# Performance work log

Measured on AMD Instinct MI355X. Metric: run time of the kernel, lower is better.

The kernel has to match this reference:

```python
import jax, jax.numpy as jnp
import numpy as np

NUM_HEADS = 16
EPS = 1e-6
CHUNK = 128  # chunk length for exact chunked-recurrent causal linear attention


def setup_inputs() -> dict:
    key = jax.random.key(0)
    ks = jax.random.split(key, 6)
    B, T, E = 4, 2048, 1024
    s = 0.02
    x = jax.random.normal(ks[0], (B, T, E), jnp.float32)
    Wq = jax.random.normal(ks[1], (E, E), jnp.float32) * s
    Wk = jax.random.normal(ks[2], (E, E), jnp.float32) * s
    Wv = jax.random.normal(ks[3], (E, E), jnp.float32) * s
    Wp = jax.random.normal(ks[4], (E, E), jnp.float32) * s
    bp = jnp.zeros((E,), jnp.float32)
    return {"x": x, "Wq": Wq, "Wk": Wk, "Wv": Wv, "Wp": Wp, "bp": bp}


def reference(x, Wq, Wk, Wv, Wp, bp):
    B, T, E = x.shape
    H = NUM_HEADS
    D = E // H
    N = T // CHUNK

    q = x @ Wq.T
    k = x @ Wk.T
    v = x @ Wv.T

    def split_heads(t):  # [B,T,E] -> [B,H,N,C,D]
        return t.reshape(B, T, H, D).transpose(0, 2, 1, 3).reshape(B, H, N, CHUNK, D)

    phi_q = jax.nn.elu(split_heads(q)) + 1.0
    phi_k = jax.nn.elu(split_heads(k)) + 1.0
    vh = split_heads(v)

    # per-chunk KV state and key-sum, then exclusive prefix over chunks
    kv = jnp.einsum('bhncd,bhnce->bhnde', phi_k, vh)        # [B,H,N,D,D]
    zk = phi_k.sum(axis=3)                                   # [B,H,N,D]
    S_prev = jnp.concatenate(
        [jnp.zeros_like(kv[:, :, :1]), jnp.cumsum(kv, axis=2)[:, :, :-1]], axis=2)
    Z_prev = jnp.concatenate(
        [jnp.zeros_like(zk[:, :, :1]), jnp.cumsum(zk, axis=2)[:, :, :-1]], axis=2)

    # intra-chunk causal part
    A = jnp.einsum('bhncd,bhnsd->bhncs', phi_q, phi_k)       # [B,H,N,C,C]
    mask = jnp.tril(jnp.ones((CHUNK, CHUNK), bool))
    A = jnp.where(mask, A, 0.0)

    num = (jnp.einsum('bhncs,bhnse->bhnce', A, vh)
           + jnp.einsum('bhncd,bhnde->bhnce', phi_q, S_prev))
    den = A.sum(-1) + jnp.einsum('bhncd,bhnd->bhnc', phi_q, Z_prev) + EPS
    y = num / den[..., None]                                  # [B,H,N,C,D]

    y = y.reshape(B, H, T, D).transpose(0, 2, 1, 3).reshape(B, T, E)
    return y @ Wp.T + bp
```

## Files before the change

kernel.cpp:

```cpp
#include <hip/hip_runtime.h>
#include <hip/hip_bf16.h>
#include <stdint.h>

#define T_LEN  2048
#define E_DIM  1024
#define BATCH  4
#define HEADS  16
#define HDIM   64
#define CHUNK_ 128
#define NCHUNK 16
#define EPS_   1e-6f

typedef __attribute__((ext_vector_type(8))) short bf16x8;
typedef __attribute__((ext_vector_type(4))) float f32x4;

__device__ __forceinline__ float b2f(__hip_bfloat16 h) { return __bfloat162float(h); }
__device__ __forceinline__ unsigned short f2bu(float f) {
  __hip_bfloat16 h = __float2bfloat16(f);
  return *(unsigned short*)&h;
}
__device__ __forceinline__ void gld_lds16(const void* g, void* l) {
  __builtin_amdgcn_global_load_lds((const __attribute__((address_space(1))) void*)g,
                                   (__attribute__((address_space(3))) void*)l,
                                   16, 0, 0);
}

__global__ __launch_bounds__(256)
void cast5(const float* __restrict__ x,  const float* __restrict__ w0,
           const float* __restrict__ w1, const float* __restrict__ w2,
           const float* __restrict__ w3,
           __hip_bfloat16* __restrict__ xb,  __hip_bfloat16* __restrict__ w0b,
           __hip_bfloat16* __restrict__ w1b, __hip_bfloat16* __restrict__ w2b,
           __hip_bfloat16* __restrict__ w3b)
{
  const int b = blockIdx.x;
  const float* s;
  __hip_bfloat16* d;
  size_t off;
  if (b < 8192) { s = x; d = xb; off = (size_t)b * 1024; }
  else {
    const int i = (b - 8192) >> 10;
    const int r = (b - 8192) & 1023;
    s = (i == 0) ? w0 : (i == 1) ? w1 : (i == 2) ? w2 : w3;
    d = (i == 0) ? w0b : (i == 1) ? w1b : (i == 2) ? w2b : w3b;
    off = (size_t)r * 1024;
  }
  const int t = threadIdx.x;
  float4 v = *(const float4*)(s + off + (size_t)t * 4);
  ushort4 o;
  o.x = f2bu(v.x); o.y = f2bu(v.y); o.z = f2bu(v.z); o.w = f2bu(v.w);
  *(ushort4*)((unsigned short*)d + off + (size_t)t * 4) = o;
}

__device__ __forceinline__ void gemm128_core(
    const __hip_bfloat16* __restrict__ X,
    const __hip_bfloat16* __restrict__ W,
    int bm, int bn, f32x4 acc[4][4],
    __hip_bfloat16* Xs, __hip_bfloat16* Ws)
{
  const int t = threadIdx.x, lane = t & 63, wave = t >> 6;
  const int wm = (wave >> 1) * 64, wn = (wave & 1) * 64;
  for (int k0 = 0; k0 < 1024; k0 += 32) {
    if (k0) __syncthreads();
#pragma unroll
    for (int i = 0; i < 2; ++i) {
      const int j = wave * 2 + i;
      const int m = j * 16 + (lane >> 2);
      const int kg = lane & 3;
      gld_lds16(X + (size_t)(bm * 128 + m) * 1024 + k0 + kg * 8, (char*)Xs + j * 1024);
      gld_lds16(W + (size_t)(bn * 128 + m) * 1024 + k0 + kg * 8, (char*)Ws + j * 1024);
    }
    __syncthreads();
    bf16x8 a[4], b[4];
#pragma unroll
    for (int i = 0; i < 4; ++i) {
      a[i] = *(const bf16x8*)&Xs[((wm + i * 16 + (lane & 15)) * 4 + (lane >> 4)) * 8];
      b[i] = *(const bf16x8*)&Ws[((wn + i * 16 + (lane & 15)) * 4 + (lane >> 4)) * 8];
    }
#pragma unroll
    for (int i = 0; i < 4; ++i)
#pragma unroll
      for (int jn = 0; jn < 4; ++jn)
        acc[i][jn] = __builtin_amdgcn_mfma_f32_16x16x32_bf16(a[i], b[jn], acc[i][jn], 0, 0, 0);
  }
}

__global__ __launch_bounds__(256, 2)
void gemm_qkv(const __hip_bfloat16* __restrict__ X,
              const __hip_bfloat16* __restrict__ Wq,
              const __hip_bfloat16* __restrict__ Wk,
              const __hip_bfloat16* __restrict__ Wv,
              __hip_bfloat16* __restrict__ qo,
              __hip_bfloat16* __restrict__ ko,
              __hip_bfloat16* __restrict__ vo)
{
  __shared__ __align__(16) __hip_bfloat16 Xs[128 * 32];
  __shared__ __align__(16) __hip_bfloat16 Ws[128 * 32];
  const int bm = blockIdx.x, bnx = blockIdx.y;
  const int which = bnx >> 3, bn = bnx & 7;
  const __hip_bfloat16* W = (which == 0) ? Wq : (which == 1) ? Wk : Wv;
  __hip_bfloat16* C = (which == 0) ? qo : (which == 1) ? ko : vo;
  const bool elu = (which < 2);
  f32x4 acc[4][4];
#pragma unroll
  for (int i = 0; i < 4; ++i)
#pragma unroll
    for (int j = 0; j < 4; ++j) acc[i][j] = (f32x4){0.f, 0.f, 0.f, 0.f};
  gemm128_core(X, W, bm, bn, acc, Xs, Ws);
  const int lane = threadIdx.x & 63, wave = threadIdx.x >> 6;
  const int wm = (wave >> 1) * 64, wn = (wave & 1) * 64;
  const int r0 = (lane >> 4) * 4;
#pragma unroll
  for (int mi = 0; mi < 4; ++mi)
#pragma unroll
    for (int ni = 0; ni < 4; ++ni) {
      const int row = bm * 128 + wm + mi * 16 + r0;
      const int col = bn * 128 + wn + ni * 16 + (lane & 15);
#pragma unroll
      for (int r = 0; r < 4; ++r) {
        float v = acc[mi][ni][r];
        if (elu) v = (v > 0.f) ? (v + 1.f) : __expf(v);
        C[(size_t)(row + r) * 1024 + col] = __float2bfloat16(v);
      }
    }
}

__global__ __launch_bounds__(256, 2)
void gemm_out(const __hip_bfloat16* __restrict__ X,
              const __hip_bfloat16* __restrict__ W,
              const float* __restrict__ bias,
              float* __restrict__ C)
{
  __shared__ __align__(16) __hip_bfloat16 Xs[128 * 32];
  __shared__ __align__(16) __hip_bfloat16 Ws[128 * 32];
  const int bm = blockIdx.x, bn = blockIdx.y;
  f32x4 acc[4][4];
#pragma unroll
  for (int i = 0; i < 4; ++i)
#pragma unroll
    for (int j = 0; j < 4; ++j) acc[i][j] = (f32x4){0.f, 0.f, 0.f, 0.f};
  gemm128_core(X, W, bm, bn, acc, Xs, Ws);
  const int lane = threadIdx.x & 63, wave = threadIdx.x >> 6;
  const int wm = (wave >> 1) * 64, wn = (wave & 1) * 64;
  const int r0 = (lane >> 4) * 4;
#pragma unroll
  for (int mi = 0; mi < 4; ++mi)
#pragma unroll
    for (int ni = 0; ni < 4; ++ni) {
      const int row = bm * 128 + wm + mi * 16 + r0;
      const int col = bn * 128 + wn + ni * 16 + (lane & 15);
      const float bv = bias[col];
#pragma unroll
      for (int r = 0; r < 4; ++r)
        C[(size_t)(row + r) * 1024 + col] = acc[mi][ni][r] + bv;
    }
}

__global__ __launch_bounds__(256)
void chunk_kv(const __hip_bfloat16* __restrict__ Kp,
              const __hip_bfloat16* __restrict__ Vp,
              float* __restrict__ kvout, float* __restrict__ zkout,
              unsigned short* __restrict__ vimg)
{
  const int bid = blockIdx.x;
  const int n = bid & 15, h = (bid >> 4) & 15, b = bid >> 8;
  __shared__ __align__(16) __hip_bfloat16 ks[CHUNK_ * HDIM];
  __shared__ __align__(16) __hip_bfloat16 vs[CHUNK_ * HDIM];
  const size_t base = ((size_t)(b * T_LEN + n * CHUNK_)) * E_DIM + h * HDIM;
  const int t = threadIdx.x;
  for (int i = t; i < CHUNK_ * 8; i += 256) {
    int r = i >> 3, c = (i & 7) << 3;
    *(uint4*)&ks[r * HDIM + c] = *(const uint4*)(Kp + base + (size_t)r * E_DIM + c);
    *(uint4*)&vs[r * HDIM + c] = *(const uint4*)(Vp + base + (size_t)r * E_DIM + c);
  }
  __syncthreads();
  const int d0 = (t >> 4) << 2, e0 = (t & 15) << 2;
  float acc[4][4] = {{0.f}};
  float z[4] = {0.f, 0.f, 0.f, 0.f};
  for (int c = 0; c < CHUNK_; ++c) {
    float kv4[4], vv4[4];
#pragma unroll
    for (int i = 0; i < 4; ++i) kv4[i] = b2f(ks[c * HDIM + d0 + i]);
#pragma unroll
    for (int j = 0; j < 4; ++j) vv4[j] = b2f(vs[c * HDIM + e0 + j]);
#pragma unroll
    for (int i = 0; i < 4; ++i) {
      z[i] += kv4[i];
#pragma unroll
      for (int j = 0; j < 4; ++j) acc[i][j] += kv4[i] * vv4[j];
    }
  }
  float* o = kvout + (size_t)bid * (HDIM * HDIM);
  const int dg = d0 >> 3, doff = d0 & 7;
#pragma unroll
  for (int i = 0; i < 4; ++i)
#pragma unroll
    for (int j = 0; j < 4; ++j)
      o[dg * 512 + (e0 + j) * 8 + doff + i] = acc[i][j];
  if (e0 == 0) {
#pragma unroll
    for (int i = 0; i < 4; ++i) zkout[(size_t)bid * HDIM + d0 + i] = z[i];
  }
  const unsigned short* vsu = (const unsigned short*)vs;
  unsigned short* vo = vimg + (size_t)bid * 8192;
  for (int slot = t; slot < 1024; slot += 256) {
    const int sg = slot >> 6, e = slot & 63;
    ushort4 lo, hi;
    lo.x = vsu[(sg * 8 + 0) * 64 + e]; lo.y = vsu[(sg * 8 + 1) * 64 + e];
    lo.z = vsu[(sg * 8 + 2) * 64 + e]; lo.w = vsu[(sg * 8 + 3) * 64 + e];
    hi.x = vsu[(sg * 8 + 4) * 64 + e]; hi.y = vsu[(sg * 8 + 5) * 64 + e];
    hi.z = vsu[(sg * 8 + 6) * 64 + e]; hi.w = vsu[(sg * 8 + 7) * 64 + e];
    *(ushort4*)&vo[slot * 8] = lo;
    *(ushort4*)&vo[slot * 8 + 4] = hi;
  }
}

__global__ __launch_bounds__(256)
void prefix_chunks(float* __restrict__ S, float* __restrict__ Z)
{
  const int bh = blockIdx.x;
  const int t = threadIdx.x;
  float run[16];
#pragma unroll
  for (int j = 0; j < 16; ++j) run[j] = 0.f;
  for (int n = 0; n < NCHUNK; ++n) {
    float* p = S + ((size_t)bh * NCHUNK + n) * (HDIM * HDIM);
#pragma unroll
    for (int j = 0; j < 16; ++j) {
      int idx = t + j * 256;
      float cur = p[idx];
      p[idx] = run[j];
      run[j] += cur;
    }
  }
  if (t < HDIM) {
    float rz = 0.f;
    for (int n = 0; n < NCHUNK; ++n) {
      float* p = Z + ((size_t)bh * NCHUNK + n) * HDIM + t;
      float cur = *p;
      *p = rz;
      rz += cur;
    }
  }
}

#define PW_STRIDE 136

__global__ __launch_bounds__(256, 3)
void chunk_attn(const __hip_bfloat16* __restrict__ Qp,
                const __hip_bfloat16* __restrict__ Kp,
                const unsigned short* __restrict__ vimg,
                const float* __restrict__ Simg,
                const float* __restrict__ Zp,
                __hip_bfloat16* __restrict__ Yp)
{
  __shared__ __align__(16) unsigned short VL[8192];
  __shared__ __align__(16) unsigned short SL[4096];
  __shared__ __align__(16) unsigned short PL[4 * 16 * PW_STRIDE];

  const int bid = blockIdx.x;
  const int n = bid & 15, h = (bid >> 4) & 15, b = bid >> 8;
  const int tokbase = b * T_LEN + n * CHUNK_;
  const size_t gbase = (size_t)tokbase * E_DIM + h * HDIM;
  const int t = threadIdx.x, lane = t & 63, wv = t >> 6;
  const int lm = lane & 15, kg = lane >> 4;

#pragma unroll
  for (int i = 0; i < 4; ++i) {
    const int j = wv * 4 + i;
    gld_lds16(vimg + (size_t)bid * 8192 + (size_t)(j * 64 + lane) * 8,
              (char*)VL + j * 1024);
  }
#pragma unroll
  for (int i = 0; i < 4; ++i) {
    const int idx = i * 1024 + t * 4;
    float4 s4 = *(const float4*)(Simg + (size_t)bid * 4096 + idx);
    ushort4 o;
    o.x = f2bu(s4.x); o.y = f2bu(s4.y); o.z = f2bu(s4.z); o.w = f2bu(s4.w);
    *(ushort4*)&SL[idx] = o;
  }

  const int mts[2] = { wv, 7 - wv };
  bf16x8 aq[2][2];
#pragma unroll
  for (int mi = 0; mi < 2; ++mi)
#pragma unroll
    for (int kh = 0; kh < 2; ++kh)
      aq[mi][kh] = *(const bf16x8*)(Qp + gbase +
                    (size_t)(mts[mi] * 16 + lm) * E_DIM + kh * 32 + kg * 8);
  bf16x8 zb[2];
#pragma unroll
  for (int kh = 0; kh < 2; ++kh) {
    float4 z0 = *(const float4*)(Zp + (size_t)bid * 64 + kh * 32 + kg * 8);
    float4 z1 = *(const float4*)(Zp + (size_t)bid * 64 + kh * 32 + kg * 8 + 4);
    zb[kh][0] = (short)f2bu(z0.x); zb[kh][1] = (short)f2bu(z0.y);
    zb[kh][2] = (short)f2bu(z0.z); zb[kh][3] = (short)f2bu(z0.w);
    zb[kh][4] = (short)f2bu(z1.x); zb[kh][5] = (short)f2bu(z1.y);
    zb[kh][6] = (short)f2bu(z1.z); zb[kh][7] = (short)f2bu(z1.w);
  }

  __syncthreads();

  f32x4 accn[2][4];
  f32x4 accden[2];
#pragma unroll
  for (int mi = 0; mi < 2; ++mi) {
    accden[mi] = (f32x4){EPS_, EPS_, EPS_, EPS_};
#pragma unroll
    for (int ne = 0; ne < 4; ++ne) accn[mi][ne] = (f32x4){0.f, 0.f, 0.f, 0.f};
  }

#pragma unroll
  for (int mi = 0; mi < 2; ++mi)
#pragma unroll
    for (int kh = 0; kh < 2; ++kh) {
      const bf16x8 a = aq[mi][kh];
      accden[mi] = __builtin_amdgcn_mfma_f32_16x16x32_bf16(a, zb[kh], accden[mi], 0, 0, 0);
#pragma unroll
      for (int ne = 0; ne < 4; ++ne) {
        bf16x8 bs = *(const bf16x8*)&SL[((kh * 4 + kg) * 64 + ne * 16 + lm) * 8];
        accn[mi][ne] = __builtin_amdgcn_mfma_f32_16x16x32_bf16(a, bs, accn[mi][ne], 0, 0, 0);
      }
    }

  unsigned short* Pw = PL + wv * 16 * PW_STRIDE;
  bf16x8 ones;
#pragma unroll
  for (int j = 0; j < 8; ++j) ones[j] = (short)0x3F80;

#pragma unroll
  for (int mi = 0; mi < 2; ++mi) {
    const int mt = mts[mi], m0 = mt * 16;
    for (int nt = 0; nt <= mt; ++nt) {
      f32x4 pt = (f32x4){0.f, 0.f, 0.f, 0.f};
#pragma unroll
      for (int kh = 0; kh < 2; ++kh) {
        bf16x8 ak = *(const bf16x8*)(Kp + gbase +
                     (size_t)(nt * 16 + lm) * E_DIM + kh * 32 + kg * 8);
        pt = __builtin_amdgcn_mfma_f32_16x16x32_bf16(ak, aq[mi][kh], pt, 0, 0, 0);
      }
      unsigned short u[4];
#pragma unroll
      for (int r = 0; r < 4; ++r) {
        float v = pt[r];
        if (nt == mt) {
          v = ((kg * 4 + r) <= lm) ? v : 0.f;
        }
        u[r] = f2bu(v);
      }
      const int sidx = lm * PW_STRIDE + nt * 16 + kg * 4;
      *(unsigned*)&Pw[sidx]     = (unsigned)u[0] | ((unsigned)u[1] << 16);
      *(unsigned*)&Pw[sidx + 2] = (unsigned)u[2] | ((unsigned)u[3] << 16);
    }
    if ((mt & 1) == 0 && lane < 32) {
      const int m = lane >> 1, half = lane & 1;
      *(uint4*)&Pw[m * PW_STRIDE + (mt + 1) * 16 + half * 8] = (uint4){0u, 0u, 0u, 0u};
    }
    const int ktc = (mt + 2) >> 1;
    for (int kt = 0; kt < ktc; ++kt) {
      bf16x8 ap = *(const bf16x8*)&Pw[lm * PW_STRIDE + kt * 32 + kg * 8];
      accden[mi] = __builtin_amdgcn_mfma_f32_16x16x32_bf16(ap, ones, accden[mi], 0, 0, 0);
#pragma unroll
      for (int ne = 0; ne < 4; ++ne) {
        bf16x8 bv = *(const bf16x8*)&VL[((kt * 4 + kg) * 64 + ne * 16 + lm) * 8];
        accn[mi][ne] = __builtin_amdgcn_mfma_f32_16x16x32_bf16(ap, bv, accn[mi][ne], 0, 0, 0);
      }
    }
  }

#pragma unroll
  for (int mi = 0; mi < 2; ++mi) {
    const int m0 = mts[mi] * 16;
    float inv[4];
#pragma unroll
    for (int r = 0; r < 4; ++r) inv[r] = 1.f / accden[mi][r];
#pragma unroll
    for (int ne = 0; ne < 4; ++ne) {
      const int col = h * HDIM + ne * 16 + lm;
#pragma unroll
      for (int r = 0; r < 4; ++r) {
        const int row = tokbase + m0 + kg * 4 + r;
        Yp[(size_t)row * E_DIM + col] = __float2bfloat16(accn[mi][ne][r] * inv[r]);
      }
    }
  }
}

extern "C" void kernel_launch(void* const* d_in, const int* in_sizes, int n_in,
                              void* d_out, int out_size, void* d_ws, size_t ws_size,
                              hipStream_t stream)
{
  const float* x  = (const float*)d_in[0];
  const float* Wq = (const float*)d_in[1];
  const float* Wk = (const float*)d_in[2];
  const float* Wv = (const float*)d_in[3];
  const float* Wp = (const float*)d_in[4];
  const float* bp = (const float*)d_in[5];
  float* out = (float*)d_out;

  const size_t MT = (size_t)BATCH * T_LEN;
  char* w = (char*)d_ws;
  __hip_bfloat16* xb  = (__hip_bfloat16*)w; w += MT * E_DIM * sizeof(__hip_bfloat16);
  __hip_bfloat16* Wqb = (__hip_bfloat16*)w; w += (size_t)E_DIM * E_DIM * sizeof(__hip_bfloat16);
  __hip_bfloat16* Wkb = (__hip_bfloat16*)w; w += (size_t)E_DIM * E_DIM * sizeof(__hip_bfloat16);
  __hip_bfloat16* Wvb = (__hip_bfloat16*)w; w += (size_t)E_DIM * E_DIM * sizeof(__hip_bfloat16);
  __hip_bfloat16* Wpb = (__hip_bfloat16*)w; w += (size_t)E_DIM * E_DIM * sizeof(__hip_bfloat16);
  __hip_bfloat16* q = (__hip_bfloat16*)w; w += MT * E_DIM * sizeof(__hip_bfloat16);
  __hip_bfloat16* k = (__hip_bfloat16*)w; w += MT * E_DIM * sizeof(__hip_bfloat16);
  __hip_bfloat16* v = (__hip_bfloat16*)w; w += MT * E_DIM * sizeof(__hip_bfloat16);
  __hip_bfloat16* y = (__hip_bfloat16*)w; w += MT * E_DIM * sizeof(__hip_bfloat16);
  float* S = (float*)w; w += (size_t)BATCH * HEADS * NCHUNK * HDIM * HDIM * sizeof(float);
  float* Z = (float*)w; w += (size_t)BATCH * HEADS * NCHUNK * HDIM * sizeof(float);
  unsigned short* vimg = (unsigned short*)xb;

  cast5<<<8192 + 4096, 256, 0, stream>>>(x, Wq, Wk, Wv, Wp, xb, Wqb, Wkb, Wvb, Wpb);
  gemm_qkv<<<dim3(MT / 128, 24), 256, 0, stream>>>(xb, Wqb, Wkb, Wvb, q, k, v);
  chunk_kv<<<BATCH * HEADS * NCHUNK, 256, 0, stream>>>(k, v, S, Z, vimg);
  prefix_chunks<<<BATCH * HEADS, 256, 0, stream>>>(S, Z);
  chunk_attn<<<BATCH * HEADS * NCHUNK, 256, 0, stream>>>(q, k, vimg, S, Z, y);
  gemm_out<<<dim3(MT / 128, 8), 256, 0, stream>>>(y, Wpb, bp, out);
}
```

Before: 246.6 us.

## Fold chunk prefix sum into attention kernel and vectorize chunk_kv LDS reads

Removes the separate prefix_chunks launch. Each chunk_attn block now sums the per-chunk KV states and key sums of all earlier chunks straight from global memory. chunk_kv also reads K/V from LDS as ushort4 vectors, converts bf16 by bit shift, and unrolls its inner loop. This drops one kernel launch and the serial prefix pass, but later chunks reread up to 15 earlier 16KB states, which adds redundant global traffic and an uneven load across blocks.

New measurement: 279.1 us. +13.2%, slower.

```diff
diff --git a/kernel.cpp b/kernel.cpp
--- a/kernel.cpp
+++ b/kernel.cpp
@@ -18,6 +18,11 @@
 __device__ __forceinline__ unsigned short f2bu(float f) {
   __hip_bfloat16 h = __float2bfloat16(f);
   return *(unsigned short*)&h;
+}
+__device__ __forceinline__ float bs2f(unsigned short v) {
+  union { unsigned int u; float f; } c;
+  c.u = ((unsigned int)v) << 16;
+  return c.f;
 }
 __device__ __forceinline__ void gld_lds16(const void* g, void* l) {
   __builtin_amdgcn_global_load_lds((const __attribute__((address_space(1))) void*)g,
@@ -175,14 +180,16 @@
   }
   __syncthreads();
   const int d0 = (t >> 4) << 2, e0 = (t & 15) << 2;
+  const unsigned short* ksu = (const unsigned short*)ks;
+  const unsigned short* vsu = (const unsigned short*)vs;
   float acc[4][4] = {{0.f}};
   float z[4] = {0.f, 0.f, 0.f, 0.f};
+#pragma unroll 4
   for (int c = 0; c < CHUNK_; ++c) {
-    float kv4[4], vv4[4];
-#pragma unroll
-    for (int i = 0; i < 4; ++i) kv4[i] = b2f(ks[c * HDIM + d0 + i]);
-#pragma unroll
-    for (int j = 0; j < 4; ++j) vv4[j] = b2f(vs[c * HDIM + e0 + j]);
+    const ushort4 ku = *(const ushort4*)&ksu[c * HDIM + d0];
+    const ushort4 vu = *(const ushort4*)&vsu[c * HDIM + e0];
+    const float kv4[4] = { bs2f(ku.x), bs2f(ku.y), bs2f(ku.z), bs2f(ku.w) };
+    const float vv4[4] = { bs2f(vu.x), bs2f(vu.y), bs2f(vu.z), bs2f(vu.w) };
 #pragma unroll
     for (int i = 0; i < 4; ++i) {
       z[i] += kv4[i];
@@ -201,7 +208,6 @@
 #pragma unroll
     for (int i = 0; i < 4; ++i) zkout[(size_t)bid * HDIM + d0 + i] = z[i];
   }
-  const unsigned short* vsu = (const unsigned short*)vs;
   unsigned short* vo = vimg + (size_t)bid * 8192;
   for (int slot = t; slot < 1024; slot += 256) {
     const int sg = slot >> 6, e = slot & 63;
@@ -215,35 +221,6 @@
   }
 }
 
-__global__ __launch_bounds__(256)
-void prefix_chunks(float* __restrict__ S, float* __restrict__ Z)
-{
-  const int bh = blockIdx.x;
-  const int t = threadIdx.x;
-  float run[16];
-#pragma unroll
-  for (int j = 0; j < 16; ++j) run[j] = 0.f;
-  for (int n = 0; n < NCHUNK; ++n) {
-    float* p = S + ((size_t)bh * NCHUNK + n) * (HDIM * HDIM);
-#pragma unroll
-    for (int j = 0; j < 16; ++j) {
-      int idx = t + j * 256;
-      float cur = p[idx];
-      p[idx] = run[j];
-      run[j] += cur;
-    }
-  }
-  if (t < HDIM) {
-    float rz = 0.f;
-    for (int n = 0; n < NCHUNK; ++n) {
-      float* p = Z + ((size_t)bh * NCHUNK + n) * HDIM + t;
-      float cur = *p;
-      *p = rz;
-      rz += cur;
-    }
-  }
-}
-
 #define PW_STRIDE 136
 
 __global__ __launch_bounds__(256, 3)
@@ -271,13 +248,20 @@
     gld_lds16(vimg + (size_t)bid * 8192 + (size_t)(j * 64 + lane) * 8,
               (char*)VL + j * 1024);
   }
-#pragma unroll
-  for (int i = 0; i < 4; ++i) {
-    const int idx = i * 1024 + t * 4;
-    float4 s4 = *(const float4*)(Simg + (size_t)bid * 4096 + idx);
-    ushort4 o;
-    o.x = f2bu(s4.x); o.y = f2bu(s4.y); o.z = f2bu(s4.z); o.w = f2bu(s4.w);
-    *(ushort4*)&SL[idx] = o;
+  {
+    const float* Sg0 = Simg + (size_t)(bid - n) * 4096;
+#pragma unroll
+    for (int i = 0; i < 4; ++i) {
+      const int idx = i * 1024 + t * 4;
+      float ax = 0.f, ay = 0.f, az = 0.f, aw = 0.f;
+      for (int m = 0; m < n; ++m) {
+        const float4 s4 = *(const float4*)(Sg0 + (size_t)m * 4096 + idx);
+        ax += s4.x; ay += s4.y; az += s4.z; aw += s4.w;
+      }
+      ushort4 o;
+      o.x = f2bu(ax); o.y = f2bu(ay); o.z = f2bu(az); o.w = f2bu(aw);
+      *(ushort4*)&SL[idx] = o;
+    }
   }
 
   const int mts[2] = { wv, 7 - wv };
@@ -291,12 +275,18 @@
   bf16x8 zb[2];
 #pragma unroll
   for (int kh = 0; kh < 2; ++kh) {
-    float4 z0 = *(const float4*)(Zp + (size_t)bid * 64 + kh * 32 + kg * 8);
-    float4 z1 = *(const float4*)(Zp + (size_t)bid * 64 + kh * 32 + kg * 8 + 4);
-    zb[kh][0] = (short)f2bu(z0.x); zb[kh][1] = (short)f2bu(z0.y);
-    zb[kh][2] = (short)f2bu(z0.z); zb[kh][3] = (short)f2bu(z0.w);
-    zb[kh][4] = (short)f2bu(z1.x); zb[kh][5] = (short)f2bu(z1.y);
-    zb[kh][6] = (short)f2bu(z1.z); zb[kh][7] = (short)f2bu(z1.w);
+    float z8[8];
+#pragma unroll
+    for (int j = 0; j < 8; ++j) z8[j] = 0.f;
+    const float* Zg0 = Zp + (size_t)(bid - n) * 64 + kh * 32 + kg * 8;
+    for (int m = 0; m < n; ++m) {
+      const float4 a0 = *(const float4*)(Zg0 + (size_t)m * 64);
+      const float4 a1 = *(const float4*)(Zg0 + (size_t)m * 64 + 4);
+      z8[0] += a0.x; z8[1] += a0.y; z8[2] += a0.z; z8[3] += a0.w;
+      z8[4] += a1.x; z8[5] += a1.y; z8[6] += a1.z; z8[7] += a1.w;
+    }
+#pragma unroll
+    for (int j = 0; j < 8; ++j) zb[kh][j] = (short)f2bu(z8[j]);
   }
 
   __syncthreads();
@@ -416,7 +406,6 @@
   cast5<<<8192 + 4096, 256, 0, stream>>>(x, Wq, Wk, Wv, Wp, xb, Wqb, Wkb, Wvb, Wpb);
   gemm_qkv<<<dim3(MT / 128, 24), 256, 0, stream>>>(xb, Wqb, Wkb, Wvb, q, k, v);
   chunk_kv<<<BATCH * HEADS * NCHUNK, 256, 0, stream>>>(k, v, S, Z, vimg);
-  prefix_chunks<<<BATCH * HEADS, 256, 0, stream>>>(S, Z);
   chunk_attn<<<BATCH * HEADS * NCHUNK, 256, 0, stream>>>(q, k, vimg, S, Z, y);
   gemm_out<<<dim3(MT / 128, 8), 256, 0, stream>>>(y, Wpb, bp, out);
 }
```
